# Performance work log

Measured on AMD Instinct MI355X. Metric: run time of the kernel, lower is better.

## Reference

```python
import jax, jax.numpy as jnp
import numpy as np

B, S, D = 4, 2048, 2048
H, KVH = 16, 4
HD = D // H            # 128
N_REP = H // KVH       # 4
SCALE = HD ** -0.5


def setup_inputs() -> dict:
    key = jax.random.key(0)
    ks = jax.random.split(key, 10)
    w = 0.02
    x = jax.random.normal(ks[0], (B, S, D), jnp.float32)
    # Linear weights stored as [in, out] (y = x @ W + b, equivalent to torch Linear)
    Wq = jax.random.normal(ks[1], (D, D), jnp.float32) * w
    bq = jnp.zeros((D,), jnp.float32)
    Wk = jax.random.normal(ks[2], (D, KVH * HD), jnp.float32) * w
    bk = jnp.zeros((KVH * HD,), jnp.float32)
    Wv = jax.random.normal(ks[3], (D, KVH * HD), jnp.float32) * w
    bv = jnp.zeros((KVH * HD,), jnp.float32)
    Wo = jax.random.normal(ks[4], (D, D), jnp.float32) * w
    bo = jnp.zeros((D,), jnp.float32)
    # RoPE tables: freqs_cis is [max_seq_len, head_dim//2] complex -> cos/sin
    inv_freq = 1.0 / (10000.0 ** (jnp.arange(0, HD, 2, dtype=jnp.float32) / HD))  # [HD//2]
    t = jnp.arange(S, dtype=jnp.float32)
    ang = jnp.outer(t, inv_freq)                     # [S, HD//2]
    freqs_cos = jnp.cos(ang)
    freqs_sin = jnp.sin(ang)
    # causal additive mask [1,1,S,S]
    neg = jnp.float32(-1e9)
    mask = jnp.where(jnp.triu(jnp.ones((S, S), bool), k=1), neg, 0.0)[None, None]
    return {"x": x, "Wq": Wq, "bq": bq, "Wk": Wk, "bk": bk, "Wv": Wv, "bv": bv,
            "Wo": Wo, "bo": bo, "freqs_cos": freqs_cos, "freqs_sin": freqs_sin,
            "mask": mask, "start_pos": 0}


def _apply_rope(q, k, cos, sin):
    # q: [B,S,H,HD], k: [B,S,KVH,HD]; interleaved complex pairs on last dim
    def rot(t):
        tr = t.reshape(*t.shape[:-1], HD // 2, 2)
        xr, xi = tr[..., 0], tr[..., 1]
        c = cos[None, :, None, :]
        s = sin[None, :, None, :]
        yr = xr * c - xi * s
        yi = xr * s + xi * c
        return jnp.stack([yr, yi], axis=-1).reshape(t.shape)
    return rot(q), rot(k)


def reference(x, Wq, bq, Wk, bk, Wv, bv, Wo, bo, freqs_cos, freqs_sin, mask, start_pos):
    Bx, Sx, _ = x.shape
    q = (x @ Wq + bq).reshape(Bx, Sx, H, HD)
    k = (x @ Wk + bk).reshape(Bx, Sx, KVH, HD)
    v = (x @ Wv + bv).reshape(Bx, Sx, KVH, HD)
    q, k = _apply_rope(q, k, freqs_cos, freqs_sin)
    # start_pos = 0 prefill: cache write-then-read is identity, so use k, v directly
    q = q.transpose(0, 2, 1, 3)                      # [B,H,S,HD]
    k = k.transpose(0, 2, 1, 3)                      # [B,KVH,S,HD]
    v = v.transpose(0, 2, 1, 3)
    k = jnp.repeat(k, N_REP, axis=1)                 # repeat_kv -> [B,H,S,HD]
    v = jnp.repeat(v, N_REP, axis=1)
    scores = jnp.einsum("bhsd,bhtd->bhst", q, k) * SCALE + mask
    w = jax.nn.softmax(scores, axis=-1)              # dropout p=0 -> identity
    out = jnp.einsum("bhst,bhtd->bhsd", w, v)
    out = out.transpose(0, 2, 1, 3).reshape(Bx, Sx, D)
    return out @ Wo + bo
```

## Files before the change

kernel.cpp:

```cpp
#include <hip/hip_runtime.h>

typedef unsigned short u16t;
typedef __bf16 bf16x8 __attribute__((ext_vector_type(8)));
typedef float f32x4 __attribute__((ext_vector_type(4)));
typedef float f32x16 __attribute__((ext_vector_type(16)));
typedef unsigned short ushort4_t __attribute__((ext_vector_type(4)));
typedef unsigned short ushort8_t __attribute__((ext_vector_type(8)));

#define B_    4
#define S_    2048
#define D_    2048
#define H_    16
#define KVH_  4
#define HD_   128
#define KDIM  2048
#define SCALE_ 0.08838834764831845f

__device__ __forceinline__ u16t f2bf(float f){
    unsigned u; __builtin_memcpy(&u, &f, 4);
    u += 0x7fffu + ((u >> 16) & 1u);
    return (u16t)(u >> 16);
}
__device__ __forceinline__ void glds16(const u16t* g, u16t* l){
    __builtin_amdgcn_global_load_lds((const __attribute__((address_space(1))) void*)g,
                                     (__attribute__((address_space(3))) void*)l, 16, 0, 0);
}
__device__ __forceinline__ void wg_barrier_lgkm(){
    __builtin_amdgcn_sched_barrier(0);
    asm volatile("s_waitcnt lgkmcnt(0)" ::: "memory");
    __builtin_amdgcn_s_barrier();
    __builtin_amdgcn_sched_barrier(0);
}
__device__ __forceinline__ void wg_barrier_vm8(){
    __builtin_amdgcn_sched_barrier(0);
    asm volatile("s_waitcnt vmcnt(8)" ::: "memory");
    __builtin_amdgcn_s_barrier();
    __builtin_amdgcn_sched_barrier(0);
}
__device__ __forceinline__ unsigned cvt_pk_bf16(float lo, float hi){
    unsigned r;
    asm("v_cvt_pk_bf16_f32 %0, %1, %2" : "=v"(r) : "v"(lo), "v"(hi));
    return r;
}
__device__ __forceinline__ void permlane32_swap(unsigned &a, unsigned &b){
    asm volatile("v_permlane32_swap_b32 %0, %1" : "+v"(a), "+v"(b));
}

__global__ void f32_to_bf16(const float* __restrict__ in, u16t* __restrict__ out)
{
    int i = (blockIdx.x * 256 + threadIdx.x) * 4;
    float4 v = *(const float4*)(in + i);
    ushort4_t p;
    p[0] = f2bf(v.x); p[1] = f2bf(v.y); p[2] = f2bf(v.z); p[3] = f2bf(v.w);
    *(ushort4_t*)(out + i) = p;
}

__global__ void transpose_f32_bf16(const float* __restrict__ W, u16t* __restrict__ Wt,
                                   int Ncols, int Krows)
{
    __shared__ u16t tile[32][33];
    int tx = threadIdx.x, ty = threadIdx.y;
    int n = blockIdx.x * 32 + tx, k = blockIdx.y * 32 + ty;
    tile[ty][tx] = f2bf(W[(size_t)k * Ncols + n]);
    __syncthreads();
    int nn = blockIdx.x * 32 + ty, kk = blockIdx.y * 32 + tx;
    Wt[(size_t)nn * Krows + kk] = tile[tx][ty];
}

#define GEMM256_PROLOGUE_AND_KLOOP(GRIDX, NWG)                                    \
    __shared__ u16t As[2][256 * 64];                                              \
    __shared__ u16t Bs[2][256 * 64];                                              \
    const int tid  = threadIdx.x;                                                 \
    const int lane = tid & 63, w = tid >> 6;                       \
    const int wm = w >> 2, wn = w & 3;                                            \
    const int lr = lane & 15, quad = lane >> 4;                                   \
    const int sx = (lr & 7) << 4;                                                 \
    const int orig = blockIdx.y * (GRIDX) + blockIdx.x;                           \
    const int lin  = (orig & 7) * ((NWG) / 8) + (orig >> 3);                      \
    const int bxs  = lin % (GRIDX), bys = lin / (GRIDX);                          \
    const int m0 = bys * 256, n0 = bxs * 256;                                     \
           \
    const int rw = w * 8 + (lane >> 3);                       \
    const int ce = ((lane & 7) ^ (lane >> 3)) * 8;          \
    f32x4 acc[8][4];                                                              \
    _Pragma("unroll")                                                             \
    for (int r = 0; r < 8; r++)                                                   \
        _Pragma("unroll")                                                         \
        for (int c = 0; c < 4; c++) acc[r][c] = (f32x4){0.f, 0.f, 0.f, 0.f};      \
                 \
    _Pragma("unroll")                                                             \
    for (int j = 0; j < 4; j++) {                                                 \
        glds16(A  + (size_t)(m0 + j * 64 + rw) * KDIM + ce,                       \
               &As[0][(j * 8 + w) * 512 + lane * 8]);                             \
        glds16(Bt + (size_t)(n0 + j * 64 + rw) * KDIM + ce,                       \
               &Bs[0][(j * 8 + w) * 512 + lane * 8]);                             \
    }                                                                             \
    _Pragma("unroll")                                                             \
    for (int j = 0; j < 4; j++) {                                                 \
        glds16(A  + (size_t)(m0 + j * 64 + rw) * KDIM + 64 + ce,                  \
               &As[1][(j * 8 + w) * 512 + lane * 8]);                             \
        glds16(Bt + (size_t)(n0 + j * 64 + rw) * KDIM + 64 + ce,                  \
               &Bs[1][(j * 8 + w) * 512 + lane * 8]);                             \
    }                                                                             \
    wg_barrier_vm8();                                                             \
    _Pragma("unroll 1")                                                           \
    for (int t = 0; t < KDIM / 64; t++) {                                         \
        const int p = t & 1;                                                      \
        const char* Ab = (const char*)&As[p][0];                                  \
        const char* Bb = (const char*)&Bs[p][0];                                  \
        bf16x8 bfr[4][2];                                                         \
        _Pragma("unroll")                                                         \
        for (int c = 0; c < 4; c++) {                                             \
            int Rb = (wn * 64 + c * 16 + lr) * 128;                               \
            bfr[c][0] = *(const bf16x8*)(Bb + ((Rb + quad * 16) ^ sx));           \
            bfr[c][1] = *(const bf16x8*)(Bb + ((Rb + 64 + quad * 16) ^ sx));      \
        }                                                                         \
        _Pragma("unroll")                                                         \
        for (int half = 0; half < 2; half++) {                                    \
            bf16x8 afr[4][2];                                                     \
            _Pragma("unroll")                                                     \
            for (int r = 0; r < 4; r++) {                                         \
                int Ra = (wm * 128 + (half * 4 + r) * 16 + lr) * 128;             \
                afr[r][0] = *(const bf16x8*)(Ab + ((Ra + quad * 16) ^ sx));       \
                afr[r][1] = *(const bf16x8*)(Ab + ((Ra + 64 + quad * 16) ^ sx));  \
            }                                                                     \
            __builtin_amdgcn_s_setprio(1);                                        \
            _Pragma("unroll")                                                     \
            for (int r = 0; r < 4; r++)                                           \
                _Pragma("unroll")                                                 \
                for (int c = 0; c < 4; c++) {                                     \
                    acc[half*4+r][c] = __builtin_amdgcn_mfma_f32_16x16x32_bf16(   \
                        afr[r][0], bfr[c][0], acc[half*4+r][c], 0, 0, 0);         \
                    acc[half*4+r][c] = __builtin_amdgcn_mfma_f32_16x16x32_bf16(   \
                        afr[r][1], bfr[c][1], acc[half*4+r][c], 0, 0, 0);         \
                }                                                                 \
            __builtin_amdgcn_s_setprio(0);                                        \
        }                                                                         \
        wg_barrier_lgkm();                       \
        const int tn = (t + 2 < KDIM / 64) ? (t + 2) : 0;     \
        const int kn = tn * 64;                                                   \
        _Pragma("unroll")                                                         \
        for (int j = 0; j < 4; j++) {                                             \
            glds16(A  + (size_t)(m0 + j * 64 + rw) * KDIM + kn + ce,              \
                   &As[p][(j * 8 + w) * 512 + lane * 8]);                         \
            glds16(Bt + (size_t)(n0 + j * 64 + rw) * KDIM + kn + ce,              \
                   &Bs[p][(j * 8 + w) * 512 + lane * 8]);                         \
        }                                                                         \
        wg_barrier_vm8();                   \
    }

__global__ __launch_bounds__(512, 2) void
gemm_o(const u16t* __restrict__ A, const u16t* __restrict__ Bt,
       const float* __restrict__ bias, float* __restrict__ out)
{
    GEMM256_PROLOGUE_AND_KLOOP(8, 256)
#pragma unroll
    for (int r = 0; r < 8; r++) {
#pragma unroll
        for (int c = 0; c < 4; c++) {
            int n = n0 + wn * 64 + c * 16 + lr;
            float bval = bias[n];
#pragma unroll
            for (int g = 0; g < 4; g++) {
                int m = m0 + wm * 128 + r * 16 + quad * 4 + g;
                out[(size_t)m * D_ + n] = acc[r][c][g] + bval;
            }
        }
    }
}

__global__ __launch_bounds__(512, 2) void
gemm_qkv(const u16t* __restrict__ A, const u16t* __restrict__ Bt,
         const float* __restrict__ bq, const float* __restrict__ bk,
         const float* __restrict__ bv,
         u16t* __restrict__ q_t, u16t* __restrict__ k_t,
         u16t* __restrict__ v_t,
         const float* __restrict__ fc, const float* __restrict__ fs)
{
    GEMM256_PROLOGUE_AND_KLOOP(12, 384)
    const int region = (bxs < 8) ? 0 : ((bxs < 10) ? 1 : 2);
#pragma unroll
    for (int r = 0; r < 8; r++) {
#pragma unroll
        for (int c = 0; c < 4; c++) {
            int n = n0 + wn * 64 + c * 16 + lr;
            if (region == 0) {
                float bval = bq[n];
                int hh = n >> 7, d = n & 127, i2 = d >> 1;
#pragma unroll
                for (int g = 0; g < 4; g++) {
                    int m = m0 + wm * 128 + r * 16 + quad * 4 + g;
                    int bb = m >> 11, s = m & (S_ - 1);
                    float v = acc[r][c][g] + bval;
                    float p = __shfl_xor(v, 1);
                    float cf = fc[s * 64 + i2], sf = fs[s * 64 + i2];
                    float o = (d & 1) ? (p * sf + v * cf) : (v * cf - p * sf);
                    q_t[(((size_t)bb * H_ + hh) * S_ + s) * HD_ + d] = f2bf(o);
                }
            } else if (region == 1) {
                int nk = n - 2048;
                float bval = bk[nk];
                int hh = nk >> 7, d = nk & 127, i2 = d >> 1;
#pragma unroll
                for (int g = 0; g < 4; g++) {
                    int m = m0 + wm * 128 + r * 16 + quad * 4 + g;
                    int bb = m >> 11, s = m & (S_ - 1);
                    float v = acc[r][c][g] + bval;
                    float p = __shfl_xor(v, 1);
                    float cf = fc[s * 64 + i2], sf = fs[s * 64 + i2];
                    float o = (d & 1) ? (p * sf + v * cf) : (v * cf - p * sf);
                    k_t[(((size_t)bb * KVH_ + hh) * S_ + s) * HD_ + d] = f2bf(o);
                }
            } else {
                int nv = n - 2560;
                float bval = bv[nv];
                int kv = nv >> 7, d = nv & 127;
                int mb = m0 + wm * 128 + r * 16 + quad * 4;
                int bb = mb >> 11, s = mb & (S_ - 1);
                ushort4_t pk;
#pragma unroll
                for (int g = 0; g < 4; g++) pk[g] = f2bf(acc[r][c][g] + bval);
                *(ushort4_t*)(v_t + (((size_t)bb * KVH_ + kv) * HD_ + d) * S_ + s) = pk;
            }
        }
    }
}

__global__ __launch_bounds__(256, 2) void
attn_kernel(const u16t* __restrict__ qt, const u16t* __restrict__ kt,
            const u16t* __restrict__ vt, u16t* __restrict__ att)
{
    __shared__ char Ks[2][8192];
    __shared__ char Vs[2][8192];
    const int tid  = threadIdx.x;
    const int lane = tid & 63, w = tid >> 6;
    const int l5 = lane & 31, hi = lane >> 5;
    const int bh = blockIdx.y, b = bh >> 4, h = bh & 15, kv = h >> 2;
    const int bx = blockIdx.x;

    const u16t* kb = kt + ((size_t)b * KVH_ + kv) * S_ * HD_;
    const u16t* vb = vt + ((size_t)b * KVH_ + kv) * HD_ * S_;

    f32x16 zero16;
#pragma unroll
    for (int j = 0; j < 16; j++) zero16[j] = 0.f;

    const int krow = tid >> 4, kcol = tid & 15;
    const int vd   = tid >> 2, vcol = tid & 3;
    const int kw0 = ((krow     ) * 256 + kcol * 16) ^ ((krow & 7) << 4);
    const int kw1 = ((krow + 16) * 256 + kcol * 16) ^ ((krow & 7) << 4);
    const int vw0 = ((vd      ) * 64 + vcol * 16) ^ (((vd >> 1) & 3) << 5);
    const int vw1 = ((vd + 64 ) * 64 + vcol * 16) ^ (((vd >> 1) & 3) << 5);

    ushort8_t kr[2][2], vr[2][2];

#pragma unroll 1
    for (int seg = 0; seg < 2; seg++) {
        const int q0 = (seg == 0 ? (15 - bx) : bx) * 128;
        const u16t* qb = qt + (((size_t)b * H_ + h) * S_ + q0) * HD_;

        bf16x8 qa[8];
#pragma unroll
        for (int ks = 0; ks < 8; ks++)
            qa[ks] = *(const bf16x8*)(qb + (w * 32 + l5) * HD_ + ks * 16 + hi * 8);

        f32x16 o[4];
#pragma unroll
        for (int i = 0; i < 4; i++) o[i] = zero16;
        float lpart = 0.f;

        const int ntile = q0 / 32 + 4;
#pragma unroll
        for (int p = 0; p < 2; p++) {
            int t0 = p * 32;
            kr[p][0] = *(const ushort8_t*)(kb + (size_t)(t0 + krow     ) * HD_ + kcol * 8);
            kr[p][1] = *(const ushort8_t*)(kb + (size_t)(t0 + krow + 16) * HD_ + kcol * 8);
            vr[p][0] = *(const ushort8_t*)(vb + (size_t)(vd     ) * S_ + t0 + vcol * 8);
            vr[p][1] = *(const ushort8_t*)(vb + (size_t)(vd + 64) * S_ + t0 + vcol * 8);
        }

        for (int it = 0; it < ntile; it += 2) {
#pragma unroll
            for (int p = 0; p < 2; p++) {
                const int t0 = (it + p) * 32;
                *(ushort8_t*)(Ks[p] + kw0) = kr[p][0];
                *(ushort8_t*)(Ks[p] + kw1) = kr[p][1];
                *(ushort8_t*)(Vs[p] + vw0) = vr[p][0];
                *(ushort8_t*)(Vs[p] + vw1) = vr[p][1];
                const int tn0 = (it + p + 2 < ntile) ? (it + p + 2) * 32 : 0;
                kr[p][0] = *(const ushort8_t*)(kb + (size_t)(tn0 + krow     ) * HD_ + kcol * 8);
                kr[p][1] = *(const ushort8_t*)(kb + (size_t)(tn0 + krow + 16) * HD_ + kcol * 8);
                vr[p][0] = *(const ushort8_t*)(vb + (size_t)(vd     ) * S_ + tn0 + vcol * 8);
                vr[p][1] = *(const ushort8_t*)(vb + (size_t)(vd + 64) * S_ + tn0 + vcol * 8);
                wg_barrier_lgkm();

                if (t0 > q0 + w * 32 + 31) continue;

                f32x16 sa = zero16, sb = zero16;
                __builtin_amdgcn_s_setprio(1);
#pragma unroll
                for (int ks = 0; ks < 8; ks += 2) {
                    bf16x8 kf0 = *(const bf16x8*)(Ks[p] +
                        ((l5 * 256 + ks * 32 + hi * 16) ^ ((l5 & 7) << 4)));
                    sa = __builtin_amdgcn_mfma_f32_32x32x16_bf16(kf0, qa[ks], sa, 0, 0, 0);
                    bf16x8 kf1 = *(const bf16x8*)(Ks[p] +
                        ((l5 * 256 + (ks + 1) * 32 + hi * 16) ^ ((l5 & 7) << 4)));
                    sb = __builtin_amdgcn_mfma_f32_32x32x16_bf16(kf1, qa[ks + 1], sb, 0, 0, 0);
                }
                __builtin_amdgcn_s_setprio(0);
                f32x16 sc = sa + sb;

                float pr[16];
                if (t0 + 31 <= q0 + w * 32) {
#pragma unroll
                    for (int r = 0; r < 16; r++) pr[r] = __expf(sc[r] * SCALE_);
                } else {
                    const int srow = q0 + w * 32 + l5;
#pragma unroll
                    for (int r = 0; r < 16; r++) {
                        int tc = t0 + (r & 3) + 8 * (r >> 2) + 4 * hi;
                        pr[r] = __expf(sc[r] * SCALE_ + ((tc > srow) ? -1e9f : 0.f));
                    }
                }
#pragma unroll
                for (int r = 0; r < 16; r++) lpart += pr[r];

                unsigned d0[4], d1[4];
#pragma unroll
                for (int q4 = 0; q4 < 4; q4++) {
                    d0[q4] = cvt_pk_bf16(pr[4 * q4 + 0], pr[4 * q4 + 1]);
                    d1[q4] = cvt_pk_bf16(pr[4 * q4 + 2], pr[4 * q4 + 3]);
                }
                permlane32_swap(d0[0], d0[1]);
                permlane32_swap(d1[0], d1[1]);
                permlane32_swap(d0[2], d0[3]);
                permlane32_swap(d1[2], d1[3]);
                union { unsigned u[4]; bf16x8 v; } pa0, pa1;
                pa0.u[0] = d0[0]; pa0.u[1] = d1[0]; pa0.u[2] = d0[1]; pa0.u[3] = d1[1];
                pa1.u[0] = d0[2]; pa1.u[1] = d1[2]; pa1.u[2] = d0[3]; pa1.u[3] = d1[3];

                __builtin_amdgcn_s_setprio(1);
#pragma unroll
                for (int dt = 0; dt < 4; dt++) {
                    bf16x8 vf0 = *(const bf16x8*)(Vs[p] +
                        (((dt * 32 + l5) * 64 + hi * 16) ^ (((l5 >> 1) & 3) << 5)));
                    o[dt] = __builtin_amdgcn_mfma_f32_32x32x16_bf16(pa0.v, vf0, o[dt], 0, 0, 0);
                    bf16x8 vf1 = *(const bf16x8*)(Vs[p] +
                        (((dt * 32 + l5) * 64 + 32 + hi * 16) ^ (((l5 >> 1) & 3) << 5)));
                    o[dt] = __builtin_amdgcn_mfma_f32_32x32x16_bf16(pa1.v, vf1, o[dt], 0, 0, 0);
                }
                __builtin_amdgcn_s_setprio(0);
            }
        }

        float lf = lpart + __shfl_xor(lpart, 32);
        float linv = 1.f / lf;
#pragma unroll
        for (int r = 0; r < 16; r++) {
            int qrow = (r & 3) + 8 * (r >> 2) + 4 * hi;
            float iv = __shfl(linv, qrow);
            int s = q0 + w * 32 + qrow;
            u16t* orow = att + ((size_t)(b * S_ + s)) * D_ + h * HD_ + l5;
#pragma unroll
            for (int dt = 0; dt < 4; dt++)
                orow[dt * 32] = f2bf(o[dt][r] * iv);
        }
    }
}

extern "C" void kernel_launch(void* const* d_in, const int* in_sizes, int n_in,
                              void* d_out, int out_size, void* d_ws, size_t ws_size,
                              hipStream_t stream)
{
    const float* x  = (const float*)d_in[0];
    const float* Wq = (const float*)d_in[1];
    const float* bq = (const float*)d_in[2];
    const float* Wk = (const float*)d_in[3];
    const float* bk = (const float*)d_in[4];
    const float* Wv = (const float*)d_in[5];
    const float* bv = (const float*)d_in[6];
    const float* Wo = (const float*)d_in[7];
    const float* bo = (const float*)d_in[8];
    const float* fc = (const float*)d_in[9];
    const float* fs = (const float*)d_in[10];

    const size_t M1 = (size_t)1024 * 1024;
    u16t* ws   = (u16t*)d_ws;
    u16t* x_bf = ws;
    u16t* att  = ws;
    u16t* Wqt  = ws + 16 * M1;
    u16t* Wot  = ws + 16 * M1;
    u16t* Wkt  = ws + 20 * M1;
    u16t* Wvt  = ws + 21 * M1;
    u16t* k_t  = ws + 22 * M1;
    u16t* v_t  = ws + 26 * M1;
    u16t* q_t  = (u16t*)d_out;

    f32_to_bf16<<<dim3(16384), 256, 0, stream>>>(x, x_bf);

    dim3 tb(32, 32);
    transpose_f32_bf16<<<dim3(64, 64), tb, 0, stream>>>(Wq, Wqt, 2048, 2048);
    transpose_f32_bf16<<<dim3(16, 64), tb, 0, stream>>>(Wk, Wkt, 512, 2048);
    transpose_f32_bf16<<<dim3(16, 64), tb, 0, stream>>>(Wv, Wvt, 512, 2048);

    gemm_qkv<<<dim3(12, 32), 512, 0, stream>>>(x_bf, Wqt, bq, bk, bv,
                                               q_t, k_t, v_t, fc, fs);

    attn_kernel<<<dim3(8, 64), 256, 0, stream>>>(q_t, k_t, v_t, att);

    transpose_f32_bf16<<<dim3(64, 64), tb, 0, stream>>>(Wo, Wot, 2048, 2048);

    gemm_o<<<dim3(8, 32), 512, 0, stream>>>(att, Wot, bo, (float*)d_out);
}
```

Before: 483.1 us.

## Restructure GEMM K-loop into eight-phase interleaved load/MFMA pipeline

The shared GEMM mainloop used by the QKV and output projections is rewritten so each K-tile is split into four MFMA phases. Between phases, each phase issues half-tile global-to-LDS loads for upcoming tiles, bracketed by barriers and priority changes. This replaces the previous scheme, which computed a full tile and then issued all next-tile loads behind a single barrier, and is meant to spread memory traffic across the compute. It adds more barriers per tile, and the buffer-reuse ordering has to stay correct for the results to be right.

```diff
diff --git a/kernel.cpp b/kernel.cpp
--- a/kernel.cpp
+++ b/kernel.cpp
@@ -14,6 +14,7 @@
 #define KVH_  4
 #define HD_   128
 #define KDIM  2048
+#define NKT   (KDIM / 64)
 #define SCALE_ 0.08838834764831845f
 
 __device__ __forceinline__ u16t f2bf(float f){
@@ -31,12 +32,6 @@
     __builtin_amdgcn_s_barrier();
     __builtin_amdgcn_sched_barrier(0);
 }
-__device__ __forceinline__ void wg_barrier_vm8(){
-    __builtin_amdgcn_sched_barrier(0);
-    asm volatile("s_waitcnt vmcnt(8)" ::: "memory");
-    __builtin_amdgcn_s_barrier();
-    __builtin_amdgcn_sched_barrier(0);
-}
 __device__ __forceinline__ unsigned cvt_pk_bf16(float lo, float hi){
     unsigned r;
     asm("v_cvt_pk_bf16_f32 %0, %1, %2" : "=v"(r) : "v"(lo), "v"(hi));
@@ -45,6 +40,7 @@
 __device__ __forceinline__ void permlane32_swap(unsigned &a, unsigned &b){
     asm volatile("v_permlane32_swap_b32 %0, %1" : "+v"(a), "+v"(b));
 }
+#define MFMA16(a, b, c) __builtin_amdgcn_mfma_f32_16x16x32_bf16((a), (b), (c), 0, 0, 0)
 
 __global__ void f32_to_bf16(const float* __restrict__ in, u16t* __restrict__ out)
 {
@@ -67,93 +63,151 @@
     Wt[(size_t)nn * Krows + kk] = tile[tx][ty];
 }
 
-#define GEMM256_PROLOGUE_AND_KLOOP(GRIDX, NWG)                                    \
-    __shared__ u16t As[2][256 * 64];                                              \
-    __shared__ u16t Bs[2][256 * 64];                                              \
+#define STAGE_HALF(G, base_off, kt, h, ldsb)                                      \
+    do {                                                                          \
+        _Pragma("unroll")                                                         \
+        for (int j_ = 0; j_ < 2; j_++) {                                          \
+            int row_ = (h) * 128 + j_ * 64 + (tid >> 3);                          \
+            glds16((G) + (size_t)((base_off) + row_) * KDIM + (kt) * 64 + sko,    \
+                   (ldsb) + row_ * 64 + (tid & 7) * 8);                           \
+        }                                                                         \
+    } while (0)
+
+#define PH_OPEN()                                                                 \
+    __builtin_amdgcn_s_barrier();                                                 \
+    asm volatile("s_waitcnt lgkmcnt(0)" ::: "memory");                            \
+    __builtin_amdgcn_sched_barrier(0);                                            \
+    __builtin_amdgcn_s_setprio(1);
+
+#define PH_CLOSE()                                                                \
+    __builtin_amdgcn_s_setprio(0);                                                \
+    __builtin_amdgcn_sched_barrier(0);                                            \
+    __builtin_amdgcn_s_barrier();
+
+#define PH_CLOSE_VM4()                                                            \
+    __builtin_amdgcn_s_setprio(0);                                                \
+    __builtin_amdgcn_sched_barrier(0);                                            \
+    asm volatile("s_waitcnt vmcnt(4)" ::: "memory");                              \
+    __builtin_amdgcn_sched_barrier(0);                                            \
+    __builtin_amdgcn_s_barrier();
+
+#define GEMM256_8P(GRIDX, NWG)                                                    \
+    __shared__ u16t Asl[2][256 * 64];                                             \
+    __shared__ u16t Bsl[2][256 * 64];                                             \
     const int tid  = threadIdx.x;                                                 \
-    const int lane = tid & 63, w = tid >> 6;                       \
+    const int lane = tid & 63, w = tid >> 6;                                      \
     const int wm = w >> 2, wn = w & 3;                                            \
     const int lr = lane & 15, quad = lane >> 4;                                   \
-    const int sx = (lr & 7) << 4;                                                 \
+    const int sx  = (lr & 7) << 4;                                                \
+    const int sko = (((tid & 7) ^ ((tid >> 3) & 7)) << 3);                        \
     const int orig = blockIdx.y * (GRIDX) + blockIdx.x;                           \
     const int lin  = (orig & 7) * ((NWG) / 8) + (orig >> 3);                      \
     const int bxs  = lin % (GRIDX), bys = lin / (GRIDX);                          \
     const int m0 = bys * 256, n0 = bxs * 256;                                     \
-           \
-    const int rw = w * 8 + (lane >> 3);                       \
-    const int ce = ((lane & 7) ^ (lane >> 3)) * 8;          \
+             \
+    STAGE_HALF(Bt, n0, 0, 0, &Bsl[0][0]);                                         \
+    STAGE_HALF(A,  m0, 0, 0, &Asl[0][0]);                                         \
+    STAGE_HALF(Bt, n0, 0, 1, &Bsl[0][0]);                                         \
+    STAGE_HALF(A,  m0, 0, 1, &Asl[0][0]);                                         \
+    STAGE_HALF(Bt, n0, 1, 0, &Bsl[1][0]);                                         \
+    STAGE_HALF(A,  m0, 1, 0, &Asl[1][0]);                                         \
     f32x4 acc[8][4];                                                              \
     _Pragma("unroll")                                                             \
     for (int r = 0; r < 8; r++)                                                   \
         _Pragma("unroll")                                                         \
         for (int c = 0; c < 4; c++) acc[r][c] = (f32x4){0.f, 0.f, 0.f, 0.f};      \
-                 \
-    _Pragma("unroll")                                                             \
-    for (int j = 0; j < 4; j++) {                                                 \
-        glds16(A  + (size_t)(m0 + j * 64 + rw) * KDIM + ce,                       \
-               &As[0][(j * 8 + w) * 512 + lane * 8]);                             \
-        glds16(Bt + (size_t)(n0 + j * 64 + rw) * KDIM + ce,                       \
-               &Bs[0][(j * 8 + w) * 512 + lane * 8]);                             \
-    }                                                                             \
-    _Pragma("unroll")                                                             \
-    for (int j = 0; j < 4; j++) {                                                 \
-        glds16(A  + (size_t)(m0 + j * 64 + rw) * KDIM + 64 + ce,                  \
-               &As[1][(j * 8 + w) * 512 + lane * 8]);                             \
-        glds16(Bt + (size_t)(n0 + j * 64 + rw) * KDIM + 64 + ce,                  \
-               &Bs[1][(j * 8 + w) * 512 + lane * 8]);                             \
-    }                                                                             \
-    wg_barrier_vm8();                                                             \
+    asm volatile("s_waitcnt vmcnt(4)" ::: "memory");                              \
+    __builtin_amdgcn_s_barrier();                                                 \
     _Pragma("unroll 1")                                                           \
-    for (int t = 0; t < KDIM / 64; t++) {                                         \
-        const int p = t & 1;                                                      \
-        const char* Ab = (const char*)&As[p][0];                                  \
-        const char* Bb = (const char*)&Bs[p][0];                                  \
-        bf16x8 bfr[4][2];                                                         \
+    for (int tt = 0; tt < NKT; tt += 2) {                                         \
         _Pragma("unroll")                                                         \
-        for (int c = 0; c < 4; c++) {                                             \
-            int Rb = (wn * 64 + c * 16 + lr) * 128;                               \
-            bfr[c][0] = *(const bf16x8*)(Bb + ((Rb + quad * 16) ^ sx));           \
-            bfr[c][1] = *(const bf16x8*)(Bb + ((Rb + 64 + quad * 16) ^ sx));      \
-        }                                                                         \
-        _Pragma("unroll")                                                         \
-        for (int half = 0; half < 2; half++) {                                    \
-            bf16x8 afr[4][2];                                                     \
+        for (int u = 0; u < 2; u++) {                                             \
+            const int t = tt + u;                                                 \
+            const char* Ab = (const char*)&Asl[u][0];                             \
+            const char* Bb = (const char*)&Bsl[u][0];                             \
+            u16t* Anb = &Asl[u ^ 1][0];                                           \
+            u16t* Bnb = &Bsl[u ^ 1][0];                                           \
+            u16t* Acb = &Asl[u][0];                                               \
+            u16t* Bcb = &Bsl[u][0];                                               \
+            const int kt1 = (t + 1 < NKT) ? t + 1 : NKT - 1;                      \
+            const int kt2 = (t + 2 < NKT) ? t + 2 : NKT - 1;                      \
+            bf16x8 a[4][2], b[4][2];                                              \
+                       \
             _Pragma("unroll")                                                     \
             for (int r = 0; r < 4; r++) {                                         \
-                int Ra = (wm * 128 + (half * 4 + r) * 16 + lr) * 128;             \
-                afr[r][0] = *(const bf16x8*)(Ab + ((Ra + quad * 16) ^ sx));       \
-                afr[r][1] = *(const bf16x8*)(Ab + ((Ra + 64 + quad * 16) ^ sx));  \
+                int Ra = (wm * 128 + r * 16 + lr) * 128;                          \
+                a[r][0] = *(const bf16x8*)(Ab + ((Ra + quad * 16) ^ sx));         \
+                a[r][1] = *(const bf16x8*)(Ab + ((Ra + 64 + quad * 16) ^ sx));    \
             }                                                                     \
-            __builtin_amdgcn_s_setprio(1);                                        \
+            _Pragma("unroll")                                                     \
+            for (int c = 0; c < 2; c++) {                                         \
+                int Rb = (wn * 64 + c * 16 + lr) * 128;                           \
+                b[c][0] = *(const bf16x8*)(Bb + ((Rb + quad * 16) ^ sx));         \
+                b[c][1] = *(const bf16x8*)(Bb + ((Rb + 64 + quad * 16) ^ sx));    \
+            }                                                                     \
+            STAGE_HALF(Bt, n0, kt1, 1, Bnb);                                      \
+            PH_OPEN()                                                             \
             _Pragma("unroll")                                                     \
             for (int r = 0; r < 4; r++)                                           \
                 _Pragma("unroll")                                                 \
-                for (int c = 0; c < 4; c++) {                                     \
-                    acc[half*4+r][c] = __builtin_amdgcn_mfma_f32_16x16x32_bf16(   \
-                        afr[r][0], bfr[c][0], acc[half*4+r][c], 0, 0, 0);         \
-                    acc[half*4+r][c] = __builtin_amdgcn_mfma_f32_16x16x32_bf16(   \
-                        afr[r][1], bfr[c][1], acc[half*4+r][c], 0, 0, 0);         \
+                for (int c = 0; c < 2; c++) {                                     \
+                    acc[r][c] = MFMA16(a[r][0], b[c][0], acc[r][c]);              \
+                    acc[r][c] = MFMA16(a[r][1], b[c][1], acc[r][c]);              \
                 }                                                                 \
-            __builtin_amdgcn_s_setprio(0);                                        \
+            PH_CLOSE()                                                            \
+                                \
+            _Pragma("unroll")                                                     \
+            for (int c = 2; c < 4; c++) {                                         \
+                int Rb = (wn * 64 + c * 16 + lr) * 128;                           \
+                b[c][0] = *(const bf16x8*)(Bb + ((Rb + quad * 16) ^ sx));         \
+                b[c][1] = *(const bf16x8*)(Bb + ((Rb + 64 + quad * 16) ^ sx));    \
+            }                                                                     \
+            STAGE_HALF(A, m0, kt1, 1, Anb);                                       \
+            PH_OPEN()                                                             \
+            _Pragma("unroll")                                                     \
+            for (int r = 0; r < 4; r++)                                           \
+                _Pragma("unroll")                                                 \
+                for (int c = 2; c < 4; c++) {                                     \
+                    acc[r][c] = MFMA16(a[r][0], b[c][0], acc[r][c]);              \
+                    acc[r][c] = MFMA16(a[r][1], b[c][1], acc[r][c]);              \
+                }                                                                 \
+            PH_CLOSE()                                                            \
+                \
+            _Pragma("unroll")                                                     \
+            for (int r = 0; r < 4; r++) {                                         \
+                int Ra = (wm * 128 + 64 + r * 16 + lr) * 128;                     \
+                a[r][0] = *(const bf16x8*)(Ab + ((Ra + quad * 16) ^ sx));         \
+                a[r][1] = *(const bf16x8*)(Ab + ((Ra + 64 + quad * 16) ^ sx));    \
+            }                                                                     \
+            STAGE_HALF(Bt, n0, kt2, 0, Bcb);                                      \
+            PH_OPEN()                                                             \
+            _Pragma("unroll")                                                     \
+            for (int r = 0; r < 4; r++)                                           \
+                _Pragma("unroll")                                                 \
+                for (int c = 0; c < 2; c++) {                                     \
+                    acc[4 + r][c] = MFMA16(a[r][0], b[c][0], acc[4 + r][c]);      \
+                    acc[4 + r][c] = MFMA16(a[r][1], b[c][1], acc[4 + r][c]);      \
+                }                                                                 \
+            PH_CLOSE()                                                            \
+                 \
+            STAGE_HALF(A, m0, kt2, 0, Acb);                                       \
+            PH_OPEN()                                                             \
+            _Pragma("unroll")                                                     \
+            for (int r = 0; r < 4; r++)                                           \
+                _Pragma("unroll")                                                 \
+                for (int c = 2; c < 4; c++) {                                     \
+                    acc[4 + r][c] = MFMA16(a[r][0], b[c][0], acc[4 + r][c]);      \
+                    acc[4 + r][c] = MFMA16(a[r][1], b[c][1], acc[4 + r][c]);      \
+                }                                                                 \
+            PH_CLOSE_VM4()                                                        \
         }                                                                         \
-        wg_barrier_lgkm();                       \
-        const int tn = (t + 2 < KDIM / 64) ? (t + 2) : 0;     \
-        const int kn = tn * 64;                                                   \
-        _Pragma("unroll")                                                         \
-        for (int j = 0; j < 4; j++) {                                             \
-            glds16(A  + (size_t)(m0 + j * 64 + rw) * KDIM + kn + ce,              \
-                   &As[p][(j * 8 + w) * 512 + lane * 8]);                         \
-            glds16(Bt + (size_t)(n0 + j * 64 + rw) * KDIM + kn + ce,              \
-                   &Bs[p][(j * 8 + w) * 512 + lane * 8]);                         \
-        }                                                                         \
-        wg_barrier_vm8();                   \
     }
 
 __global__ __launch_bounds__(512, 2) void
 gemm_o(const u16t* __restrict__ A, const u16t* __restrict__ Bt,
        const float* __restrict__ bias, float* __restrict__ out)
 {
-    GEMM256_PROLOGUE_AND_KLOOP(8, 256)
+    GEMM256_8P(8, 256)
 #pragma unroll
     for (int r = 0; r < 8; r++) {
 #pragma unroll
@@ -177,7 +231,7 @@
          u16t* __restrict__ v_t,
          const float* __restrict__ fc, const float* __restrict__ fs)
 {
-    GEMM256_PROLOGUE_AND_KLOOP(12, 384)
+    GEMM256_8P(12, 384)
     const int region = (bxs < 8) ? 0 : ((bxs < 10) ? 1 : 2);
 #pragma unroll
     for (int r = 0; r < 8; r++) {
@@ -315,11 +369,11 @@
 #pragma unroll
                     for (int r = 0; r < 16; r++) pr[r] = __expf(sc[r] * SCALE_);
                 } else {
-                    const int srow = q0 + w * 32 + l5;
+                    const int srow2 = q0 + w * 32 + l5;
 #pragma unroll
                     for (int r = 0; r < 16; r++) {
                         int tc = t0 + (r & 3) + 8 * (r >> 2) + 4 * hi;
-                        pr[r] = __expf(sc[r] * SCALE_ + ((tc > srow) ? -1e9f : 0.f));
+                        pr[r] = __expf(sc[r] * SCALE_ + ((tc > srow2) ? -1e9f : 0.f));
                     }
                 }
 #pragma unroll
```

After: 543.9 us. +12.6%, slower.
